# Kernel tuning notes

Hardware: AMD Instinct MI355X
Metric: run time of the kernel (lower is better)

The kernel has to match this reference:

```python
import jax, jax.numpy as jnp
import numpy as np

GRID_MIN, GRID_MAX = -3.0, 3.0
N_AXIS = 64            # 64x64 grid -> m = 4096
LENGTHSCALE = 0.5      # RBF kernel lengthscale
EPS = 1e-6


def make_grid():
    lin = jnp.linspace(GRID_MIN, GRID_MAX, N_AXIS, dtype=jnp.float32)
    gx, gy = jnp.meshgrid(lin, lin, indexing='ij')
    return jnp.stack([gx.ravel(), gy.ravel()], axis=-1)  # [m, 2]


def setup_inputs() -> dict:
    key = jax.random.key(0)
    k1, k2 = jax.random.split(key)
    X = jax.random.normal(k1, (16, 1024, 2), dtype=jnp.float32)  # context locations
    Y = jax.random.normal(k2, (16, 1024, 8), dtype=jnp.float32)  # context values
    return {"X": X, "Y": Y}


def reference(X, Y):
    grid = make_grid()                                   # [m, 2]
    # expand_with_ones: prepend a ones channel (density channel)
    ones = jnp.ones(Y.shape[:-1] + (1,), dtype=Y.dtype)
    Yb = jnp.concatenate([ones, Y], axis=-1)             # [b, n, 1+dy]

    # kernel_smooth: RBF kernel between grid and X, contracted with Yb.
    # squared distances via the expanded form (avoids [b,m,n,2] intermediate)
    g2 = jnp.sum(grid * grid, axis=-1)                   # [m]
    x2 = jnp.sum(X * X, axis=-1)                         # [b, n]
    gx = jnp.einsum('md,bnd->bmn', grid, X)              # [b, m, n]
    d2 = g2[None, :, None] + x2[:, None, :] - 2.0 * gx   # [b, m, n]
    K = jnp.exp(-d2 / (2.0 * LENGTHSCALE * LENGTHSCALE)) # [b, m, n]

    Y_grid = jnp.einsum('bmn,bnc->bmc', K, Yb)           # [b, m, 1+dy]

    # normalise: divide feature channels by the density channel
    density = Y_grid[:, :, :1]
    feats = Y_grid[:, :, 1:] / (density + EPS)
    Y_grid = jnp.concatenate([density, feats], axis=-1)

    return grid[None], Y_grid
```

## Files before the change

### kernel.cpp

```cpp
#include <hip/hip_runtime.h>

typedef _Float16 half8   __attribute__((ext_vector_type(8)));
typedef float    floatx4 __attribute__((ext_vector_type(4)));

#define STEP  (6.0f / 63.0f)
#define SCAL  1.69864636f

#define EYF_SZ (16 * 65536)
#define EXF_SZ (16 * 65536)
#define YBF_SZ (16 * 16384)

__global__ __launch_bounds__(256) void rkhs_tables(
    const float* __restrict__ X, const float* __restrict__ Y,
    _Float16* __restrict__ EyF, _Float16* __restrict__ ExF,
    _Float16* __restrict__ YbF)
{
    const int gid = blockIdx.x * 256 + threadIdx.x;
    if (gid < 131072) {
        const int n = gid & 15, q = (gid >> 4) & 3, ct = (gid >> 6) & 3,
                  s = (gid >> 8) & 31, b = gid >> 13;
        const int col = ct * 16 + n, k0 = s * 32 + q * 8;
        const float gS = SCAL * (-3.0f + (float)col * STEP);
        half8 h;
#pragma unroll
        for (int j = 0; j < 8; ++j) {
            const float x = X[(((b << 10) + k0 + j) << 1) + 1];
            const float d = fmaf(-SCAL, x, gS);
            h[j] = (_Float16)__builtin_amdgcn_exp2f(-(d * d));
        }
        *(half8*)(EyF + (size_t)gid * 8) = h;
    } else if (gid < 262144) {
        const int u = gid - 131072;
        const int qq = u & 3, r = (u >> 2) & 63, s = (u >> 8) & 31, b = u >> 13;
        const int k0 = s * 32 + qq * 8;
        const float gS = SCAL * (-3.0f + (float)r * STEP);
        half8 h;
#pragma unroll
        for (int j = 0; j < 8; ++j) {
            const float x = X[(((b << 10) + k0 + j) << 1)];
            const float d = fmaf(-SCAL, x, gS);
            h[j] = (_Float16)__builtin_amdgcn_exp2f(-(d * d));
        }
        *(half8*)(ExF + (size_t)u * 8) = h;
    } else {
        const int v = gid - 262144;
        const int n = v & 15, q = (v >> 4) & 3, s = (v >> 6) & 31, b = v >> 11;
        const int k0 = s * 32 + q * 8;
        half8 h;
#pragma unroll
        for (int j = 0; j < 8; ++j) {
            float val = 0.f;
            if (n == 0)      val = 1.f;
            else if (n <= 8) val = Y[(((b << 10) + k0 + j) << 3) + n - 1];
            h[j] = (_Float16)val;
        }
        *(half8*)(YbF + (size_t)v * 8) = h;
    }
}

__global__ __launch_bounds__(512, 2) void rkhs_gemm(
    const _Float16* __restrict__ EyF, const _Float16* __restrict__ ExF,
    const _Float16* __restrict__ YbF, float* __restrict__ out)
{
    __shared__ floatx4 spark[4096];
    float* sfin = (float*)spark;

    const int b   = blockIdx.x >> 4;
    const int rw  = blockIdx.x & 15;
    const int tid = threadIdx.x;
    const int kq  = tid >> 6, l = tid & 63, q = l >> 4, n = l & 15;
    const int r0  = rw * 4;

    if (b == 0) {
        const int row = r0 + (tid >> 7), rem = tid & 127;
        out[(size_t)rw * 512 + tid] = (rem & 1)
            ? (-3.0f + (float)(rem >> 1) * STEP)
            : (-3.0f + (float)row * STEP);
    }

    floatx4 acc[4][4];
#pragma unroll
    for (int rr = 0; rr < 4; ++rr)
#pragma unroll
        for (int ct = 0; ct < 4; ++ct) acc[rr][ct] = (floatx4){0.f, 0.f, 0.f, 0.f};

#pragma unroll
    for (int ss = 0; ss < 4; ++ss) {
        const int s = kq * 4 + ss;
        const size_t sb = (size_t)(b * 32 + s);
        const half8 yb = *(const half8*)(YbF + (sb * 64 + l) * 8);
        half8 bp[4];
#pragma unroll
        for (int rr = 0; rr < 4; ++rr) {
            const half8 ex = *(const half8*)(ExF + (sb * 64 + r0 + rr) * 32 + q * 8);
            bp[rr] = ex * yb;
        }
#pragma unroll
        for (int ct = 0; ct < 4; ++ct) {
            const half8 ey = *(const half8*)(EyF + ((sb * 4 + ct) * 64 + l) * 8);
#pragma unroll
            for (int rr = 0; rr < 4; ++rr)
                acc[rr][ct] = __builtin_amdgcn_mfma_f32_16x16x32_f16(ey, bp[rr], acc[rr][ct], 0, 0, 0);
        }
    }

#define PARKA(slot)                                                        \
    { _Pragma("unroll") for (int rr = 0; rr < 4; ++rr)                     \
      _Pragma("unroll") for (int ct = 0; ct < 4; ++ct)                     \
          spark[(slot) * 1024 + (rr * 4 + ct) * 64 + l] = acc[rr][ct]; }
#define ABSORBA(slot)                                                      \
    { _Pragma("unroll") for (int rr = 0; rr < 4; ++rr)                     \
      _Pragma("unroll") for (int ct = 0; ct < 4; ++ct)                     \
          acc[rr][ct] += spark[(slot) * 1024 + (rr * 4 + ct) * 64 + l]; }

    if (kq >= 4) PARKA(kq - 4)
    __syncthreads();
    if (kq < 4)  ABSORBA(kq)
    __syncthreads();
    if (kq == 2 || kq == 3) PARKA(kq - 2)
    __syncthreads();
    if (kq < 2)  ABSORBA(kq)
    __syncthreads();
    if (kq == 1) PARKA(0)
    __syncthreads();

    if (kq == 0) {
        ABSORBA(0)
#pragma unroll
        for (int rr = 0; rr < 4; ++rr)
#pragma unroll
            for (int ct = 0; ct < 4; ++ct)
                if (n < 9)
#pragma unroll
                    for (int i = 0; i < 4; ++i)
                        sfin[(rr * 64 + ct * 16 + q * 4 + i) * 9 + n] = acc[rr][ct][i];
    }
#undef PARKA
#undef ABSORBA
    __syncthreads();

    const size_t obase = 8192 + ((size_t)b * 4096 + (size_t)r0 * 64) * 9;
#pragma unroll
    for (int it = 0; it < 5; ++it) {
        const int idx = it * 512 + tid;
        if (idx < 2304) {
            const int m  = idx / 9;
            const int ch = idx - m * 9;
            const float dens = sfin[m * 9];
            const float v    = sfin[idx];
            out[obase + idx] = ch ? v * __builtin_amdgcn_rcpf(dens + 1e-6f) : dens;
        }
    }
}

extern "C" void kernel_launch(void* const* d_in, const int* in_sizes, int n_in,
                              void* d_out, int out_size, void* d_ws, size_t ws_size,
                              hipStream_t stream) {
    const float* X = (const float*)d_in[0];
    const float* Y = (const float*)d_in[1];
    float* out = (float*)d_out;

    _Float16* EyF = (_Float16*)d_ws;
    _Float16* ExF = EyF + EYF_SZ;
    _Float16* YbF = ExF + EXF_SZ;

    rkhs_tables<<<dim3(1152), dim3(256), 0, stream>>>(X, Y, EyF, ExF, YbF);
    rkhs_gemm  <<<dim3(256),  dim3(512), 0, stream>>>(EyF, ExF, YbF, out);
}
```

Before: 67.58 us.

## Fuse table precompute into GEMM kernel, computing exp factors in LDS per chunk

Replaces the separate table-building kernel and the global fp16 workspace with a single fused kernel. Each block stages X and Y for a 256-point chunk into shared memory, computes the separable RBF factors (Ex, Ey) and the padded Yb tile in LDS, then runs the MFMA accumulation from LDS. This removes a kernel launch and the global write and re-read of about 4.5 MB of tables. In exchange, each of the 16 row-blocks per batch recomputes the full Ey table, and extra barriers per chunk serialize compute with the MFMA phase. The 64 KB of shared memory per block may limit occupancy.

```diff
diff --git a/kernel.cpp b/kernel.cpp
--- a/kernel.cpp
+++ b/kernel.cpp
@@ -6,69 +6,24 @@
 #define STEP  (6.0f / 63.0f)
 #define SCAL  1.69864636f
 
-#define EYF_SZ (16 * 65536)
-#define EXF_SZ (16 * 65536)
-#define YBF_SZ (16 * 16384)
-
-__global__ __launch_bounds__(256) void rkhs_tables(
-    const float* __restrict__ X, const float* __restrict__ Y,
-    _Float16* __restrict__ EyF, _Float16* __restrict__ ExF,
-    _Float16* __restrict__ YbF)
+__global__ __launch_bounds__(512, 2) void rkhs_fused(
+    const float* __restrict__ X,
+    const float* __restrict__ Y,
+    float* __restrict__ out)
 {
-    const int gid = blockIdx.x * 256 + threadIdx.x;
-    if (gid < 131072) {
-        const int n = gid & 15, q = (gid >> 4) & 3, ct = (gid >> 6) & 3,
-                  s = (gid >> 8) & 31, b = gid >> 13;
-        const int col = ct * 16 + n, k0 = s * 32 + q * 8;
-        const float gS = SCAL * (-3.0f + (float)col * STEP);
-        half8 h;
-#pragma unroll
-        for (int j = 0; j < 8; ++j) {
-            const float x = X[(((b << 10) + k0 + j) << 1) + 1];
-            const float d = fmaf(-SCAL, x, gS);
-            h[j] = (_Float16)__builtin_amdgcn_exp2f(-(d * d));
-        }
-        *(half8*)(EyF + (size_t)gid * 8) = h;
-    } else if (gid < 262144) {
-        const int u = gid - 131072;
-        const int qq = u & 3, r = (u >> 2) & 63, s = (u >> 8) & 31, b = u >> 13;
-        const int k0 = s * 32 + qq * 8;
-        const float gS = SCAL * (-3.0f + (float)r * STEP);
-        half8 h;
-#pragma unroll
-        for (int j = 0; j < 8; ++j) {
-            const float x = X[(((b << 10) + k0 + j) << 1)];
-            const float d = fmaf(-SCAL, x, gS);
-            h[j] = (_Float16)__builtin_amdgcn_exp2f(-(d * d));
-        }
-        *(half8*)(ExF + (size_t)u * 8) = h;
-    } else {
-        const int v = gid - 262144;
-        const int n = v & 15, q = (v >> 4) & 3, s = (v >> 6) & 31, b = v >> 11;
-        const int k0 = s * 32 + q * 8;
-        half8 h;
-#pragma unroll
-        for (int j = 0; j < 8; ++j) {
-            float val = 0.f;
-            if (n == 0)      val = 1.f;
-            else if (n <= 8) val = Y[(((b << 10) + k0 + j) << 3) + n - 1];
-            h[j] = (_Float16)val;
-        }
-        *(half8*)(YbF + (size_t)v * 8) = h;
-    }
-}
-
-__global__ __launch_bounds__(512, 2) void rkhs_gemm(
-    const _Float16* __restrict__ EyF, const _Float16* __restrict__ ExF,
-    const _Float16* __restrict__ YbF, float* __restrict__ out)
-{
-    __shared__ floatx4 spark[4096];
-    float* sfin = (float*)spark;
+    __shared__ __align__(16) unsigned char smem[65536];
+    float2*   sX    = (float2*)smem;
+    float*    sYf   = (float*)(smem + 2048);
+    _Float16* sEx   = (_Float16*)(smem + 10240);
+    _Float16* sYb   = (_Float16*)(smem + 12288);
+    _Float16* sEy   = (_Float16*)(smem + 20480);
+    floatx4*  spark = (floatx4*)smem;
+    float*    sfin  = (float*)smem;
 
     const int b   = blockIdx.x >> 4;
     const int rw  = blockIdx.x & 15;
     const int tid = threadIdx.x;
-    const int kq  = tid >> 6, l = tid & 63, q = l >> 4, n = l & 15;
+    const int w   = tid >> 6, l = tid & 63, q = l >> 4, n = l & 15;
     const int r0  = rw * 4;
 
     if (b == 0) {
@@ -84,25 +39,72 @@
 #pragma unroll
         for (int ct = 0; ct < 4; ++ct) acc[rr][ct] = (floatx4){0.f, 0.f, 0.f, 0.f};
 
+    for (int c = 0; c < 4; ++c) {
+        const int kb = c * 256;
+        __syncthreads();
+        if (tid < 256)
+            sX[tid] = ((const float2*)X)[b * 1024 + kb + tid];
+        ((float4*)sYf)[tid] =
+            ((const float4*)(Y + ((size_t)b * 1024 + kb) * 8))[tid];
+        __syncthreads();
+
+        if (tid < 128) {
+            const int s_loc = tid >> 4, rr = (tid >> 2) & 3, qq = tid & 3;
+            const int kk = s_loc * 32 + qq * 8;
+            const float gS = SCAL * (-3.0f + (float)(r0 + rr) * STEP);
+            half8 h;
 #pragma unroll
-    for (int ss = 0; ss < 4; ++ss) {
-        const int s = kq * 4 + ss;
-        const size_t sb = (size_t)(b * 32 + s);
-        const half8 yb = *(const half8*)(YbF + (sb * 64 + l) * 8);
-        half8 bp[4];
+            for (int j = 0; j < 8; ++j) {
+                const float d = fmaf(-SCAL, sX[kk + j].x, gS);
+                h[j] = (_Float16)__builtin_amdgcn_exp2f(-(d * d));
+            }
+            *(half8*)(sEx + (s_loc * 4 + rr) * 32 + qq * 8) = h;
+        }
+        {
+            const int kk = w * 32 + q * 8;
+            half8 h;
 #pragma unroll
-        for (int rr = 0; rr < 4; ++rr) {
-            const half8 ex = *(const half8*)(ExF + (sb * 64 + r0 + rr) * 32 + q * 8);
-            bp[rr] = ex * yb;
+            for (int j = 0; j < 8; ++j) {
+                float v = 0.f;
+                if (n == 0)      v = 1.f;
+                else if (n <= 8) v = sYf[(kk + j) * 8 + n - 1];
+                h[j] = (_Float16)v;
+            }
+            *(half8*)(sYb + (w * 64 + l) * 8) = h;
         }
 #pragma unroll
-        for (int ct = 0; ct < 4; ++ct) {
-            const half8 ey = *(const half8*)(EyF + ((sb * 4 + ct) * 64 + l) * 8);
+        for (int i = 0; i < 4; ++i) {
+            const int u = tid + 512 * i;
+            const int ll = u & 63;
+            const int kk = ((u >> 8) & 7) * 32 + (ll >> 4) * 8;
+            const int col = ((u >> 6) & 3) * 16 + (ll & 15);
+            const float gS = SCAL * (-3.0f + (float)col * STEP);
+            half8 h;
+#pragma unroll
+            for (int j = 0; j < 8; ++j) {
+                const float d = fmaf(-SCAL, sX[kk + j].y, gS);
+                h[j] = (_Float16)__builtin_amdgcn_exp2f(-(d * d));
+            }
+            *(half8*)(sEy + (size_t)u * 8) = h;
+        }
+        __syncthreads();
+
+        {
+            const half8 yb = *(const half8*)(sYb + (w * 64 + l) * 8);
+            half8 bp[4];
 #pragma unroll
             for (int rr = 0; rr < 4; ++rr)
-                acc[rr][ct] = __builtin_amdgcn_mfma_f32_16x16x32_f16(ey, bp[rr], acc[rr][ct], 0, 0, 0);
+                bp[rr] = (*(const half8*)(sEx + (w * 4 + rr) * 32 + q * 8)) * yb;
+#pragma unroll
+            for (int ct = 0; ct < 4; ++ct) {
+                const half8 ey = *(const half8*)(sEy + ((w * 4 + ct) * 64 + l) * 8);
+#pragma unroll
+                for (int rr = 0; rr < 4; ++rr)
+                    acc[rr][ct] = __builtin_amdgcn_mfma_f32_16x16x32_f16(ey, bp[rr], acc[rr][ct], 0, 0, 0);
+            }
         }
     }
+    __syncthreads();
 
 #define PARKA(slot)                                                        \
     { _Pragma("unroll") for (int rr = 0; rr < 4; ++rr)                     \
@@ -113,18 +115,18 @@
       _Pragma("unroll") for (int ct = 0; ct < 4; ++ct)                     \
           acc[rr][ct] += spark[(slot) * 1024 + (rr * 4 + ct) * 64 + l]; }
 
-    if (kq >= 4) PARKA(kq - 4)
+    if (w >= 4) PARKA(w - 4)
     __syncthreads();
-    if (kq < 4)  ABSORBA(kq)
+    if (w < 4)  ABSORBA(w)
     __syncthreads();
-    if (kq == 2 || kq == 3) PARKA(kq - 2)
+    if (w == 2 || w == 3) PARKA(w - 2)
     __syncthreads();
-    if (kq < 2)  ABSORBA(kq)
+    if (w < 2)  ABSORBA(w)
     __syncthreads();
-    if (kq == 1) PARKA(0)
+    if (w == 1) PARKA(0)
     __syncthreads();
 
-    if (kq == 0) {
+    if (w == 0) {
         ABSORBA(0)
 #pragma unroll
         for (int rr = 0; rr < 4; ++rr)
@@ -160,10 +162,5 @@
     const float* Y = (const float*)d_in[1];
     float* out = (float*)d_out;
 
-    _Float16* EyF = (_Float16*)d_ws;
-    _Float16* ExF = EyF + EYF_SZ;
-    _Float16* YbF = ExF + EXF_SZ;
-
-    rkhs_tables<<<dim3(1152), dim3(256), 0, stream>>>(X, Y, EyF, ExF, YbF);
-    rkhs_gemm  <<<dim3(256),  dim3(512), 0, stream>>>(EyF, ExF, YbF, out);
+    rkhs_fused<<<dim3(256), dim3(512), 0, stream>>>(X, Y, out);
 }
```

New measurement: 65.98 us. -2.4%, faster.
